# Kernel optimization log

Measured on AMD Instinct MI355X. Metric: run time of the kernel, lower is better.

## Reference

```python
import jax, jax.numpy as jnp
import numpy as np

B, T, V, D = 2048, 32, 1024, 256


def setup_inputs() -> dict:
    key = jax.random.key(0)
    k1, k2 = jax.random.split(key)
    input = jax.random.normal(k1, (B, T, D), dtype=jnp.float32)
    codebook = jax.random.normal(k2, (T, V, D), dtype=jnp.float32)
    return {"input": input, "codebook": codebook}


def reference(input, codebook):
    # input: [B, T, D]; codebook: [T, V, D]
    x = jnp.moveaxis(input, 1, 0)  # [T, B, D]
    # Squared euclidean distances; argmin is invariant to the sqrt in cdist.
    x2 = jnp.sum(x * x, axis=-1)[..., None]            # [T, B, 1]
    c2 = jnp.sum(codebook * codebook, axis=-1)[:, None, :]  # [T, 1, V]
    xc = jnp.einsum('tbd,tvd->tbv', x, codebook)       # [T, B, V]
    d2 = x2 - 2.0 * xc + c2                            # [T, B, V]
    idxes_ = jnp.argmin(d2, axis=-1)                   # [T, B]
    idxes = idxes_.T                                   # [B, T]
    # Direct per-token gather: embed[b, t] = codebook[t, idxes[b, t]]
    embed_ = codebook[jnp.arange(T)[:, None], idxes_]  # [T, B, D]
    embed = jnp.moveaxis(embed_, 0, 1)                 # [B, T, D]
    return embed, idxes
```

## Files before the change

### kernel.cpp

```cpp
#include <hip/hip_runtime.h>
#include <hip/hip_bf16.h>


#define B_ 2048
#define T_ 32
#define V_ 1024
#define D_ 256

#define BT 128
#define VT 128
#define NVT (V_ / VT)
#define CAND_MAX 512
#define MARGIN 8.0f

typedef __attribute__((ext_vector_type(8))) short short8;
typedef __attribute__((ext_vector_type(4))) float f32x4;

__device__ __forceinline__ unsigned short f2bf(float f) {
    unsigned u = __builtin_bit_cast(unsigned, f);
    unsigned r = u + 0x7FFFu + ((u >> 16) & 1u);
    return (unsigned short)(r >> 16);
}

__device__ __forceinline__ short8 pack8(float4 a, float4 b) {
    short8 r;
    r[0] = (short)f2bf(a.x); r[1] = (short)f2bf(a.y);
    r[2] = (short)f2bf(a.z); r[3] = (short)f2bf(a.w);
    r[4] = (short)f2bf(b.x); r[5] = (short)f2bf(b.y);
    r[6] = (short)f2bf(b.z); r[7] = (short)f2bf(b.w);
    return r;
}

__global__ void c2_kernel(const float* __restrict__ cb, float* __restrict__ c2) {
    int row  = blockIdx.x * 4 + (threadIdx.x >> 6);
    int lane = threadIdx.x & 63;
    const float4 v = ((const float4*)(cb + (size_t)row * D_))[lane];
    float s = v.x * v.x + v.y * v.y + v.z * v.z + v.w * v.w;
    #pragma unroll
    for (int off = 32; off > 0; off >>= 1) s += __shfl_down(s, off, 64);
    if (lane == 0) c2[row] = s;
}

__global__ __launch_bounds__(256, 2)
void vq_kernel(const float* __restrict__ x, const float* __restrict__ cb,
               const float* __restrict__ c2, float* __restrict__ out) {
    const int t  = blockIdx.x;
    const int b0 = blockIdx.y * BT;

    __shared__ short8 A_lds[4096];
    __shared__ short8 Bc_lds[640];
    __shared__ float  minPart[BT * 2];
    __shared__ float  minS[BT];
    __shared__ unsigned long long result[BT];
    __shared__ unsigned s_cand[CAND_MAX];
    __shared__ unsigned s_cnt;
    __shared__ int    IdxS[BT];

    const int tid  = threadIdx.x;
    const int wave = tid >> 6, lane = tid & 63;
    const int wm = wave & 1, wn = wave >> 1;
    const int q  = lane >> 4, ln = lane & 15;

    if (tid < BT) result[tid] = ~0ULL;
    if (tid == 0) s_cnt = 0;

    #pragma unroll
    for (int i = 0; i < 16; ++i) {
        int gid = i * 256 + tid;
        int r = gid >> 5, g = gid & 31;
        const float4* src = (const float4*)(x + (((size_t)(b0 + r)) * T_ + t) * D_ + g * 8);
        A_lds[r * 32 + (g ^ (r & 15))] = pack8(src[0], src[1]);
    }

    auto stage_B = [&](int vt, int kc) {
        #pragma unroll
        for (int i = 0; i < 2; ++i) {
            int gid = i * 256 + tid;
            int r = gid >> 2, g = gid & 3;
            const float4* src = (const float4*)(cb + ((size_t)t * V_ + vt * VT + r) * D_ + kc * 32 + g * 8);
            Bc_lds[r * 5 + g] = pack8(src[0], src[1]);
        }
    };

    auto mfma_vt = [&](int vt, f32x4 (&acc)[4][4]) {
        #pragma unroll
        for (int mt = 0; mt < 4; ++mt)
            #pragma unroll
            for (int nt = 0; nt < 4; ++nt) acc[mt][nt] = (f32x4){0.f, 0.f, 0.f, 0.f};
        for (int kc = 0; kc < 8; ++kc) {
            __syncthreads();
            stage_B(vt, kc);
            __syncthreads();
            short8 af[4], bf[4];
            #pragma unroll
            for (int mt = 0; mt < 4; ++mt) {
                int m = wm * 64 + mt * 16 + ln;
                af[mt] = A_lds[m * 32 + ((kc * 4 + q) ^ ln)];
            }
            #pragma unroll
            for (int nt = 0; nt < 4; ++nt) {
                int n = wn * 64 + nt * 16 + ln;
                bf[nt] = Bc_lds[n * 5 + q];
            }
            #pragma unroll
            for (int mt = 0; mt < 4; ++mt)
                #pragma unroll
                for (int nt = 0; nt < 4; ++nt)
                    acc[mt][nt] = __builtin_amdgcn_mfma_f32_16x16x32_bf16(af[mt], bf[nt], acc[mt][nt], 0, 0, 0);
        }
    };

    float runmin[16];
    #pragma unroll
    for (int s = 0; s < 16; ++s) runmin[s] = 3.4e38f;

    for (int vt = 0; vt < NVT; ++vt) {
        f32x4 acc[4][4];
        mfma_vt(vt, acc);
        const float* c2p = c2 + t * V_ + vt * VT + wn * 64 + ln;
        #pragma unroll
        for (int nt = 0; nt < 4; ++nt) {
            const float cc = c2p[nt * 16];
            #pragma unroll
            for (int mt = 0; mt < 4; ++mt)
                #pragma unroll
                for (int i = 0; i < 4; ++i) {
                    float s = fmaf(-2.0f, acc[mt][nt][i], cc);
                    runmin[mt * 4 + i] = fminf(runmin[mt * 4 + i], s);
                }
        }
    }

    #pragma unroll
    for (int s = 0; s < 16; ++s) {
        float v = runmin[s];
        v = fminf(v, __shfl_xor(v, 1, 64));
        v = fminf(v, __shfl_xor(v, 2, 64));
        v = fminf(v, __shfl_xor(v, 4, 64));
        v = fminf(v, __shfl_xor(v, 8, 64));
        runmin[s] = v;
    }
    if (ln == 0) {
        #pragma unroll
        for (int s = 0; s < 16; ++s) {
            int row = wm * 64 + (s >> 2) * 16 + q * 4 + (s & 3);
            minPart[row * 2 + wn] = runmin[s];
        }
    }
    __syncthreads();
    if (tid < BT) minS[tid] = fminf(minPart[tid * 2], minPart[tid * 2 + 1]) + MARGIN;
    __syncthreads();
    float thr[16];
    #pragma unroll
    for (int s = 0; s < 16; ++s)
        thr[s] = minS[wm * 64 + (s >> 2) * 16 + q * 4 + (s & 3)];

    for (int vt = 0; vt < NVT; ++vt) {
        f32x4 acc[4][4];
        mfma_vt(vt, acc);
        const float* c2p = c2 + t * V_ + vt * VT + wn * 64 + ln;
        #pragma unroll
        for (int nt = 0; nt < 4; ++nt) {
            const float cc = c2p[nt * 16];
            const int v = vt * VT + wn * 64 + nt * 16 + ln;
            #pragma unroll
            for (int mt = 0; mt < 4; ++mt)
                #pragma unroll
                for (int i = 0; i < 4; ++i) {
                    float s = fmaf(-2.0f, acc[mt][nt][i], cc);
                    if (s < thr[mt * 4 + i]) {
                        int row = wm * 64 + mt * 16 + q * 4 + i;
                        unsigned pos = atomicAdd(&s_cnt, 1u);
                        if (pos < CAND_MAX) s_cand[pos] = (unsigned)((row << 10) | v);
                    }
                }
        }
    }

    __syncthreads();
    const unsigned ncand = min(s_cnt, (unsigned)CAND_MAX);
    const int grp = tid >> 4, l16 = tid & 15;
    for (unsigned ci = grp; ci < ncand; ci += 16) {
        const unsigned e = s_cand[ci];
        const int row = e >> 10, v = e & 1023;
        const float* xr = x + (((size_t)(b0 + row)) * T_ + t) * D_ + l16 * 16;
        const float* cr = cb + ((size_t)t * V_ + v) * D_ + l16 * 16;
        float dot = 0.f;
        #pragma unroll
        for (int j = 0; j < 4; ++j) {
            float4 a = *(const float4*)(xr + j * 4);
            float4 b = *(const float4*)(cr + j * 4);
            dot = fmaf(a.x, b.x, dot); dot = fmaf(a.y, b.y, dot);
            dot = fmaf(a.z, b.z, dot); dot = fmaf(a.w, b.w, dot);
        }
        dot += __shfl_xor(dot, 1, 64);
        dot += __shfl_xor(dot, 2, 64);
        dot += __shfl_xor(dot, 4, 64);
        dot += __shfl_xor(dot, 8, 64);
        if (l16 == 0) {
            float sc = fmaf(-2.0f, dot, c2[t * V_ + v]);
            unsigned u = __builtin_bit_cast(unsigned, sc);
            u = (u & 0x80000000u) ? ~u : (u | 0x80000000u);
            unsigned long long pk = ((unsigned long long)u << 32) | (unsigned)v;
            atomicMin(&result[row], pk);
        }
    }
    __syncthreads();

    if (tid < BT) {
        const int idx = (int)(result[tid] & 0xFFFFFFFFull);
        IdxS[tid] = idx;
        out[(size_t)B_ * T_ * D_ + (size_t)(b0 + tid) * T_ + t] = (float)idx;
    }
    __syncthreads();

    const int w = tid >> 6, gl = tid & 63;
    #pragma unroll
    for (int i = 0; i < 32; ++i) {
        const int row = w * 32 + i;
        const int idx = IdxS[row];
        const float4 src = *(const float4*)(cb + ((size_t)t * V_ + idx) * D_ + gl * 4);
        *(float4*)(out + (((size_t)(b0 + row)) * T_ + t) * D_ + gl * 4) = src;
    }
}

extern "C" void kernel_launch(void* const* d_in, const int* in_sizes, int n_in,
                              void* d_out, int out_size, void* d_ws, size_t ws_size,
                              hipStream_t stream) {
    const float* x  = (const float*)d_in[0];
    const float* cb = (const float*)d_in[1];
    float* out = (float*)d_out;
    float* c2  = (float*)d_ws;

    c2_kernel<<<dim3(T_ * V_ / 4), 256, 0, stream>>>(cb, c2);
    vq_kernel<<<dim3(T_, B_ / BT), 256, 0, stream>>>(x, cb, c2, out);
}
```

Before: 285.8 us.

## Fuse VQ min and candidate passes into one GEMM sweep with pre-swizzled bf16 codebook

Replaces the two full GEMM sweeps (one for the running minimum, one to collect near-minimum candidates) with a single sweep. Candidates are now filtered against the running minimum so far, which is looser, so the candidate buffer grows to 1280 entries. A prep kernel converts the codebook to swizzled bf16 tiles once per call. Those tiles are streamed into LDS with global_load_lds, and the next tile is staged while MFMAs run. The cost is a prep kernel writing 16MB, extra fp32 rescoring work from more candidates, and overflow risk in the candidate buffer, which could give wrong argmins.

Measured after the change: 281.9 us. Within noise of the previous version (-1.3%).

```diff
diff --git a/kernel.cpp b/kernel.cpp
--- a/kernel.cpp
+++ b/kernel.cpp
@@ -6,11 +6,10 @@
 #define T_ 32
 #define V_ 1024
 #define D_ 256
-
 #define BT 128
 #define VT 128
-#define NVT (V_ / VT)
-#define CAND_MAX 512
+#define NVT 8
+#define CAND_MAX 1280
 #define MARGIN 8.0f
 
 typedef __attribute__((ext_vector_type(8))) short short8;
@@ -31,67 +30,101 @@
     return r;
 }
 
+__device__ __forceinline__ void load_lds16(const void* g, void* l) {
+    __builtin_amdgcn_global_load_lds(
+        (const __attribute__((address_space(1))) unsigned int*)g,
+        (__attribute__((address_space(3))) unsigned int*)l, 16, 0, 0);
+}
+
+__global__ void prep_kernel(const float* __restrict__ cb, float* __restrict__ c2,
+                            unsigned short* __restrict__ cbs) {
+    const int wave = threadIdx.x >> 6, lane = threadIdx.x & 63;
+    const int row = blockIdx.x * 4 + wave;
+    const float4 v4 = *(const float4*)(cb + (size_t)row * D_ + lane * 4);
+    float s = v4.x * v4.x + v4.y * v4.y + v4.z * v4.z + v4.w * v4.w;
+    #pragma unroll
+    for (int off = 32; off; off >>= 1) s += __shfl_down(s, off, 64);
+    if (lane == 0) c2[row] = s;
+
+    ushort4 b4;
+    b4.x = f2bf(v4.x); b4.y = f2bf(v4.y); b4.z = f2bf(v4.z); b4.w = f2bf(v4.w);
+    const int t = row >> 10, v = row & 1023, vt = v >> 7, r7 = v & 127;
+    const int kc = lane >> 3, g = (lane >> 1) & 3, half = lane & 1;
+    const size_t off_us = ((size_t)((t * NVT + vt) * 8 + kc)) * 4096
+                        + (size_t)(r7 * 4 + (g ^ (r7 & 3))) * 8 + half * 4;
+    *(ushort4*)(cbs + off_us) = b4;
+}
+
 __global__ void c2_kernel(const float* __restrict__ cb, float* __restrict__ c2) {
-    int row  = blockIdx.x * 4 + (threadIdx.x >> 6);
-    int lane = threadIdx.x & 63;
+    const int row = blockIdx.x * 4 + (threadIdx.x >> 6);
+    const int lane = threadIdx.x & 63;
     const float4 v = ((const float4*)(cb + (size_t)row * D_))[lane];
     float s = v.x * v.x + v.y * v.y + v.z * v.z + v.w * v.w;
     #pragma unroll
-    for (int off = 32; off > 0; off >>= 1) s += __shfl_down(s, off, 64);
+    for (int off = 32; off; off >>= 1) s += __shfl_down(s, off, 64);
     if (lane == 0) c2[row] = s;
 }
 
 __global__ __launch_bounds__(256, 2)
 void vq_kernel(const float* __restrict__ x, const float* __restrict__ cb,
-               const float* __restrict__ c2, float* __restrict__ out) {
+               const float* __restrict__ c2, const unsigned short* __restrict__ cbs,
+               float* __restrict__ out, int use_swz) {
     const int t  = blockIdx.x;
     const int b0 = blockIdx.y * BT;
 
     __shared__ short8 A_lds[4096];
-    __shared__ short8 Bc_lds[640];
+    __shared__ short8 B_lds[512];
     __shared__ float  minPart[BT * 2];
-    __shared__ float  minS[BT];
     __shared__ unsigned long long result[BT];
     __shared__ unsigned s_cand[CAND_MAX];
     __shared__ unsigned s_cnt;
-    __shared__ int    IdxS[BT];
-
-    const int tid  = threadIdx.x;
+
+    const int tid = threadIdx.x;
     const int wave = tid >> 6, lane = tid & 63;
     const int wm = wave & 1, wn = wave >> 1;
-    const int q  = lane >> 4, ln = lane & 15;
+    const int q = lane >> 4, ln = lane & 15;
 
     if (tid < BT) result[tid] = ~0ULL;
+    minPart[tid] = 3.4e38f;
     if (tid == 0) s_cnt = 0;
 
     #pragma unroll
     for (int i = 0; i < 16; ++i) {
-        int gid = i * 256 + tid;
-        int r = gid >> 5, g = gid & 31;
+        int gid = i * 256 + tid, r = gid >> 5, g = gid & 31;
         const float4* src = (const float4*)(x + (((size_t)(b0 + r)) * T_ + t) * D_ + g * 8);
         A_lds[r * 32 + (g ^ (r & 15))] = pack8(src[0], src[1]);
     }
 
     auto stage_B = [&](int vt, int kc) {
-        #pragma unroll
-        for (int i = 0; i < 2; ++i) {
-            int gid = i * 256 + tid;
-            int r = gid >> 2, g = gid & 3;
-            const float4* src = (const float4*)(cb + ((size_t)t * V_ + vt * VT + r) * D_ + kc * 32 + g * 8);
-            Bc_lds[r * 5 + g] = pack8(src[0], src[1]);
+        if (use_swz) {
+            const unsigned short* tile = cbs + ((size_t)((t * NVT + vt) * 8 + kc)) * 4096;
+            #pragma unroll
+            for (int i = 0; i < 2; ++i) {
+                const int gr = wave * 128 + i * 64;
+                load_lds16(tile + (size_t)(gr + lane) * 8, (void*)(B_lds + gr));
+            }
+        } else {
+            #pragma unroll
+            for (int i = 0; i < 2; ++i) {
+                int gid = i * 256 + tid, r = gid >> 2, g = gid & 3;
+                const float4* src = (const float4*)(cb + ((size_t)t * V_ + vt * VT + r) * D_ + kc * 32 + g * 8);
+                B_lds[r * 4 + (g ^ (r & 3))] = pack8(src[0], src[1]);
+            }
         }
     };
 
-    auto mfma_vt = [&](int vt, f32x4 (&acc)[4][4]) {
+    stage_B(0, 0);
+    __syncthreads();
+
+    for (int vt = 0; vt < NVT; ++vt) {
+        f32x4 acc[4][4];
         #pragma unroll
         for (int mt = 0; mt < 4; ++mt)
             #pragma unroll
             for (int nt = 0; nt < 4; ++nt) acc[mt][nt] = (f32x4){0.f, 0.f, 0.f, 0.f};
+
         for (int kc = 0; kc < 8; ++kc) {
-            __syncthreads();
-            stage_B(vt, kc);
-            __syncthreads();
-            short8 af[4], bf[4];
+            short8 af[4], bfr[4];
             #pragma unroll
             for (int mt = 0; mt < 4; ++mt) {
                 int m = wm * 64 + mt * 16 + ln;
@@ -100,81 +133,63 @@
             #pragma unroll
             for (int nt = 0; nt < 4; ++nt) {
                 int n = wn * 64 + nt * 16 + ln;
-                bf[nt] = Bc_lds[n * 5 + q];
+                bfr[nt] = B_lds[n * 4 + (q ^ (n & 3))];
+            }
+            __syncthreads();
+            if (!(vt == NVT - 1 && kc == 7)) {
+                int nk = kc + 1, nv = vt;
+                if (nk == 8) { nk = 0; nv = vt + 1; }
+                stage_B(nv, nk);
             }
             #pragma unroll
             for (int mt = 0; mt < 4; ++mt)
                 #pragma unroll
                 for (int nt = 0; nt < 4; ++nt)
-                    acc[mt][nt] = __builtin_amdgcn_mfma_f32_16x16x32_bf16(af[mt], bf[nt], acc[mt][nt], 0, 0, 0);
-        }
-    };
-
-    float runmin[16];
-    #pragma unroll
-    for (int s = 0; s < 16; ++s) runmin[s] = 3.4e38f;
-
-    for (int vt = 0; vt < NVT; ++vt) {
-        f32x4 acc[4][4];
-        mfma_vt(vt, acc);
+                    acc[mt][nt] = __builtin_amdgcn_mfma_f32_16x16x32_bf16(af[mt], bfr[nt], acc[mt][nt], 0, 0, 0);
+            __syncthreads();
+        }
+
         const float* c2p = c2 + t * V_ + vt * VT + wn * 64 + ln;
-        #pragma unroll
-        for (int nt = 0; nt < 4; ++nt) {
-            const float cc = c2p[nt * 16];
-            #pragma unroll
-            for (int mt = 0; mt < 4; ++mt)
+        float cc[4];
+        #pragma unroll
+        for (int nt = 0; nt < 4; ++nt) cc[nt] = c2p[nt * 16];
+
+        #pragma unroll
+        for (int mt = 0; mt < 4; ++mt)
+            #pragma unroll
+            for (int i = 0; i < 4; ++i) {
+                float mn = 3.4e38f;
                 #pragma unroll
-                for (int i = 0; i < 4; ++i) {
-                    float s = fmaf(-2.0f, acc[mt][nt][i], cc);
-                    runmin[mt * 4 + i] = fminf(runmin[mt * 4 + i], s);
+                for (int nt = 0; nt < 4; ++nt)
+                    mn = fminf(mn, fmaf(-2.0f, acc[mt][nt][i], cc[nt]));
+                mn = fminf(mn, __shfl_xor(mn, 1, 64));
+                mn = fminf(mn, __shfl_xor(mn, 2, 64));
+                mn = fminf(mn, __shfl_xor(mn, 4, 64));
+                mn = fminf(mn, __shfl_xor(mn, 8, 64));
+                if (ln == 0) {
+                    int r = wm * 64 + mt * 16 + q * 4 + i;
+                    minPart[r * 2 + wn] = fminf(minPart[r * 2 + wn], mn);
                 }
-        }
-    }
-
-    #pragma unroll
-    for (int s = 0; s < 16; ++s) {
-        float v = runmin[s];
-        v = fminf(v, __shfl_xor(v, 1, 64));
-        v = fminf(v, __shfl_xor(v, 2, 64));
-        v = fminf(v, __shfl_xor(v, 4, 64));
-        v = fminf(v, __shfl_xor(v, 8, 64));
-        runmin[s] = v;
-    }
-    if (ln == 0) {
-        #pragma unroll
-        for (int s = 0; s < 16; ++s) {
-            int row = wm * 64 + (s >> 2) * 16 + q * 4 + (s & 3);
-            minPart[row * 2 + wn] = runmin[s];
-        }
-    }
-    __syncthreads();
-    if (tid < BT) minS[tid] = fminf(minPart[tid * 2], minPart[tid * 2 + 1]) + MARGIN;
-    __syncthreads();
-    float thr[16];
-    #pragma unroll
-    for (int s = 0; s < 16; ++s)
-        thr[s] = minS[wm * 64 + (s >> 2) * 16 + q * 4 + (s & 3)];
-
-    for (int vt = 0; vt < NVT; ++vt) {
-        f32x4 acc[4][4];
-        mfma_vt(vt, acc);
-        const float* c2p = c2 + t * V_ + vt * VT + wn * 64 + ln;
-        #pragma unroll
-        for (int nt = 0; nt < 4; ++nt) {
-            const float cc = c2p[nt * 16];
-            const int v = vt * VT + wn * 64 + nt * 16 + ln;
-            #pragma unroll
-            for (int mt = 0; mt < 4; ++mt)
+            }
+        __syncthreads();
+
+        #pragma unroll
+        for (int mt = 0; mt < 4; ++mt)
+            #pragma unroll
+            for (int i = 0; i < 4; ++i) {
+                int r = wm * 64 + mt * 16 + q * 4 + i;
+                float2 mp = *(const float2*)&minPart[r * 2];
+                float thr = fminf(mp.x, mp.y) + MARGIN;
                 #pragma unroll
-                for (int i = 0; i < 4; ++i) {
-                    float s = fmaf(-2.0f, acc[mt][nt][i], cc);
-                    if (s < thr[mt * 4 + i]) {
-                        int row = wm * 64 + mt * 16 + q * 4 + i;
+                for (int nt = 0; nt < 4; ++nt) {
+                    float s = fmaf(-2.0f, acc[mt][nt][i], cc[nt]);
+                    if (s < thr) {
+                        int v = vt * VT + wn * 64 + nt * 16 + ln;
                         unsigned pos = atomicAdd(&s_cnt, 1u);
-                        if (pos < CAND_MAX) s_cand[pos] = (unsigned)((row << 10) | v);
+                        if (pos < CAND_MAX) s_cand[pos] = (unsigned)((r << 10) | v);
                     }
                 }
-        }
+            }
     }
 
     __syncthreads();
@@ -201,24 +216,20 @@
             float sc = fmaf(-2.0f, dot, c2[t * V_ + v]);
             unsigned u = __builtin_bit_cast(unsigned, sc);
             u = (u & 0x80000000u) ? ~u : (u | 0x80000000u);
-            unsigned long long pk = ((unsigned long long)u << 32) | (unsigned)v;
-            atomicMin(&result[row], pk);
+            atomicMin(&result[row], ((unsigned long long)u << 32) | (unsigned)v);
         }
     }
     __syncthreads();
 
-    if (tid < BT) {
-        const int idx = (int)(result[tid] & 0xFFFFFFFFull);
-        IdxS[tid] = idx;
-        out[(size_t)B_ * T_ * D_ + (size_t)(b0 + tid) * T_ + t] = (float)idx;
-    }
-    __syncthreads();
+    if (tid < BT)
+        out[(size_t)B_ * T_ * D_ + (size_t)(b0 + tid) * T_ + t] =
+            (float)(int)(result[tid] & 1023u);
 
     const int w = tid >> 6, gl = tid & 63;
     #pragma unroll
     for (int i = 0; i < 32; ++i) {
         const int row = w * 32 + i;
-        const int idx = IdxS[row];
+        const int idx = (int)(result[row] & 1023u);
         const float4 src = *(const float4*)(cb + ((size_t)t * V_ + idx) * D_ + gl * 4);
         *(float4*)(out + (((size_t)(b0 + row)) * T_ + t) * D_ + gl * 4) = src;
     }
@@ -231,7 +242,11 @@
     const float* cb = (const float*)d_in[1];
     float* out = (float*)d_out;
     float* c2  = (float*)d_ws;
-
-    c2_kernel<<<dim3(T_ * V_ / 4), 256, 0, stream>>>(cb, c2);
-    vq_kernel<<<dim3(T_, B_ / BT), 256, 0, stream>>>(x, cb, c2, out);
-}
+    unsigned short* cbs = (unsigned short*)((char*)d_ws + 131072);
+    const size_t NEED = 131072 + (size_t)T_ * V_ * D_ * 2;
+    const int use_swz = (ws_size >= NEED) ? 1 : 0;
+
+    if (use_swz) prep_kernel<<<dim3(T_ * V_ / 4), 256, 0, stream>>>(cb, c2, cbs);
+    else         c2_kernel<<<dim3(T_ * V_ / 4), 256, 0, stream>>>(cb, c2);
+    vq_kernel<<<dim3(T_, B_ / BT), 256, 0, stream>>>(x, cb, c2, cbs, out, use_swz);
+}
```
